# Kernel tuning notes

Hardware: AMD Instinct MI355X
Metric: run time of the kernel (lower is better)

The kernel has to match this reference:

```python
import jax, jax.numpy as jnp
import numpy as np

DIM = 512
NUM_HEADS = 16
D_HEAD = DIM // NUM_HEADS
B, S = 4, 1024


def _relative_shift(pos_score):
    # pos_score: [B, H, S1, S2] -> Transformer-XL relative shift
    b, h, s1, s2 = pos_score.shape
    padded = jnp.pad(pos_score, ((0, 0), (0, 0), (0, 0), (1, 0)))  # [B,H,S1,S2+1]
    padded = padded.reshape(b, h, s2 + 1, s1)
    return padded[:, :, 1:].reshape(b, h, s1, s2)


def setup_inputs() -> dict:
    key = jax.random.key(0)
    ks = jax.random.split(key, 16)
    f32 = jnp.float32
    scale = 0.02
    inp = {
        "query": jax.random.normal(ks[0], (B, S, DIM), f32),
        "key": jax.random.normal(ks[1], (B, S, DIM), f32),
        "value": jax.random.normal(ks[2], (B, S, DIM), f32),
        "pos_embedding": jax.random.normal(ks[3], (B, S, DIM), f32),
        "Wq": jax.random.normal(ks[4], (DIM, DIM), f32) * scale,
        "bq": jnp.zeros((DIM,), f32),
        "Wk": jax.random.normal(ks[5], (DIM, DIM), f32) * scale,
        "bk": jnp.zeros((DIM,), f32),
        "Wv": jax.random.normal(ks[6], (DIM, DIM), f32) * scale,
        "bv": jnp.zeros((DIM,), f32),
        "Wp": jax.random.normal(ks[7], (DIM, DIM), f32) * scale,  # pos_proj, no bias
        "u_bias": jax.random.normal(ks[8], (NUM_HEADS, D_HEAD), f32) * scale,
        "v_bias": jax.random.normal(ks[9], (NUM_HEADS, D_HEAD), f32) * scale,
        "Wo": jax.random.normal(ks[10], (DIM, DIM), f32) * scale,
        "bo": jnp.zeros((DIM,), f32),
    }
    return inp


def reference(query, key, value, pos_embedding, Wq, bq, Wk, bk, Wv, bv, Wp,
              u_bias, v_bias, Wo, bo):
    b = query.shape[0]
    # projections (torch Linear: x @ W.T + b), split heads -> [B, S, H, Dh]
    q = (query @ Wq.T + bq).reshape(b, -1, NUM_HEADS, D_HEAD)
    k = (key @ Wk.T + bk).reshape(b, -1, NUM_HEADS, D_HEAD)
    v = (value @ Wv.T + bv).reshape(b, -1, NUM_HEADS, D_HEAD)
    p = (pos_embedding @ Wp.T).reshape(b, -1, NUM_HEADS, D_HEAD)

    # content score: (q + u) @ k^T  -> [B, H, Sq, Sk]
    content_score = jnp.einsum('bqhd,bkhd->bhqk', q + u_bias, k)
    # position score: (q + v) @ pos^T, then relative shift
    pos_score = jnp.einsum('bqhd,bkhd->bhqk', q + v_bias, p)
    pos_score = _relative_shift(pos_score)

    score = (content_score + pos_score) / np.sqrt(D_HEAD).astype(np.float32)
    attn = jax.nn.softmax(score, axis=-1)  # dropout_p = 0.0 -> identity

    context = jnp.einsum('bhqk,bkhd->bqhd', attn, v).reshape(b, -1, DIM)
    return context @ Wo.T + bo
```

## Files before the change

### kernel.cpp

```cpp
#include <hip/hip_runtime.h>
#include <hip/hip_bf16.h>
#include <math.h>


typedef float f32x4 __attribute__((ext_vector_type(4)));
typedef __bf16 bf16x8 __attribute__((ext_vector_type(8)));
typedef __bf16 bf16x2 __attribute__((ext_vector_type(2)));

#define MFMA16(a, b, c) __builtin_amdgcn_mfma_f32_16x16x32_bf16((a), (b), (c), 0, 0, 0)

constexpr int Bb  = 4;
constexpr int S   = 1024;
constexpr int H   = 16;
constexpr int Dh  = 32;
constexpr int DIM = 512;
constexpr float SCALEL2E = 0.25501818637084186f;
constexpr int ZROWS = 3 * S + 16;

constexpr size_t XN = (size_t)Bb * S * DIM;
constexpr size_t WN = (size_t)DIM * DIM;

__device__ inline bf16x8 cvt8(const float* __restrict__ p) {
  f32x4 a = *(const f32x4*)p;
  f32x4 b = *(const f32x4*)(p + 4);
  bf16x8 r;
  r[0] = (__bf16)a[0]; r[1] = (__bf16)a[1]; r[2] = (__bf16)a[2]; r[3] = (__bf16)a[3];
  r[4] = (__bf16)b[0]; r[5] = (__bf16)b[1]; r[6] = (__bf16)b[2]; r[7] = (__bf16)b[3];
  return r;
}

__device__ inline float fexp2(float x) {
  float r;
  asm("v_exp_f32 %0, %1" : "=v"(r) : "v"(x));
  return r;
}

__device__ inline void gload_lds16(const __bf16* g, __bf16* l) {
  __builtin_amdgcn_global_load_lds(
      (const __attribute__((address_space(1))) unsigned int*)g,
      (__attribute__((address_space(3))) unsigned int*)l, 16, 0, 0);
}

__global__ __launch_bounds__(256) void conv_kernel(
    const float* __restrict__ q, const float* __restrict__ k,
    const float* __restrict__ v, const float* __restrict__ p,
    const float* __restrict__ wq, const float* __restrict__ wk,
    const float* __restrict__ wv, const float* __restrict__ wp,
    const float* __restrict__ wo,
    __bf16* __restrict__ xb, __bf16* __restrict__ wb,
    __bf16* __restrict__ phZ)
{
  const int y = blockIdx.y;
  if (y == 9) {
    const int e8 = blockIdx.x * 256 + threadIdx.x;
    if (e8 < 64 * 136 * 4) {
      const int rowIdx = e8 >> 2, chunk = e8 & 3;
      const int bh = rowIdx / 136;
      const int rl = rowIdx - bh * 136;
      const int row = (rl < 72) ? (960 + rl) : (2040 + (rl - 72));
      bf16x8 zz = {};
      *(bf16x8*)(phZ + ((size_t)bh * ZROWS + row) * Dh + chunk * 8) = zz;
    }
    return;
  }
  const float* src;
  size_t n;
  __bf16* dst;
  if (y < 4) {
    src = (y == 0) ? q : (y == 1) ? k : (y == 2) ? v : p;
    n = XN;
    dst = xb + (size_t)y * XN;
  } else {
    const int w = y - 4;
    src = (w == 0) ? wq : (w == 1) ? wk : (w == 2) ? wv : (w == 3) ? wp : wo;
    n = WN;
    dst = wb + (size_t)w * WN;
  }
  const size_t i = ((size_t)blockIdx.x * 256 + threadIdx.x) * 8;
  if (i >= n) return;
  *(bf16x8*)(dst + i) = cvt8(src + i);
}

template <int MODE>
__global__ __launch_bounds__(256) void gemm_kernel(
    const __bf16* __restrict__ xb, const __bf16* __restrict__ wb,
    const __bf16* __restrict__ ctxp,
    const float* __restrict__ bq, const float* __restrict__ bk,
    const float* __restrict__ bv, const float* __restrict__ bo,
    const float* __restrict__ ub, const float* __restrict__ vb,
    __bf16* __restrict__ qu, __bf16* __restrict__ qv,
    __bf16* __restrict__ kk, __bf16* __restrict__ vt,
    __bf16* __restrict__ phZ,
    float* __restrict__ outp)
{
  constexpr int MR = 2;
  constexpr int BM = MR * 32;
  __shared__ __align__(16) __bf16 smem[BM * 64 + 128 * 64];
  __bf16* As = smem;
  __bf16* Bs = smem + BM * 64;
  __bf16* trans = smem;

  const int bid = blockIdx.x;
  const int u = bid >> 3;
  const int by = u & 3;
  const int idx = (bid & 7) + 8 * (u >> 2);
  int bx, z;
  if (MODE == 0) { bx = idx & 63; z = idx >> 6; }
  else           { bx = idx;      z = 4; }

  const __bf16* Ag = (z < 4) ? (xb + (size_t)z * XN) : ctxp;
  const __bf16* Bg = wb + (size_t)z * WN;

  const int tid = threadIdx.x;
  const int wid = tid >> 6;
  const int ln = tid & 63;
  const int lm = ln & 15, lg = ln >> 4;
  const int wr = wid >> 1, wc = wid & 1;
  const int brow = bx * BM;
  const int bcol = by * 128;

  const int srow = ln >> 3;
  const int sc   = ln & 7;

  f32x4 acc[MR][4] = {};

  for (int kt = 0; kt < DIM / 64; ++kt) {
    const int k0 = kt * 64;
#pragma unroll
    for (int i = 0; i < MR; ++i) {
      const int rb = wid * (MR * 8) + i * 8;
      const int r = rb + srow;
      const int cg = sc ^ (r & 7);
      gload_lds16(Ag + (size_t)(brow + r) * DIM + k0 + cg * 8, &As[rb * 64]);
    }
#pragma unroll
    for (int i = 0; i < 4; ++i) {
      const int rb = wid * 32 + i * 8;
      const int r = rb + srow;
      const int cg = sc ^ (r & 7);
      gload_lds16(Bg + (size_t)(bcol + r) * DIM + k0 + cg * 8, &Bs[rb * 64]);
    }
    __syncthreads();

#pragma unroll
    for (int ks = 0; ks < 2; ++ks) {
      bf16x8 a[MR], b[4];
#pragma unroll
      for (int m = 0; m < MR; ++m) {
        const int row = wr * (MR * 16) + m * 16 + lm;
        const int cc = (ks * 4 + lg) ^ (row & 7);
        a[m] = *(const bf16x8*)&As[row * 64 + cc * 8];
      }
#pragma unroll
      for (int n = 0; n < 4; ++n) {
        const int row = wc * 64 + n * 16 + lm;
        const int cc = (ks * 4 + lg) ^ (row & 7);
        b[n] = *(const bf16x8*)&Bs[row * 64 + cc * 8];
      }
#pragma unroll
      for (int m = 0; m < MR; ++m)
#pragma unroll
        for (int n = 0; n < 4; ++n)
          acc[m][n] = MFMA16(a[m], b[n], acc[m][n]);
    }
    __syncthreads();
  }

  if (MODE == 0 && z == 2) {
    const int b = brow >> 10;
    const int sbase = brow & (S - 1);
#pragma unroll
    for (int n = 0; n < 4; ++n) {
      const int dl = wc * 64 + n * 16 + lm;
      const float bias = bv[bcol + dl];
#pragma unroll
      for (int r = 0; r < 4; ++r) {
        const int p = wr * 32 + 2 * (lg * 4 + r);
        bf16x2 pk;
        pk[0] = (__bf16)(acc[0][n][r] + bias);
        pk[1] = (__bf16)(acc[1][n][r] + bias);
        const int base = dl * 64 + (((p >> 3) ^ (dl & 7)) * 8) + (p & 7);
        *(bf16x2*)(trans + base) = pk;
      }
    }
    __syncthreads();
#pragma unroll
    for (int j = 0; j < 2; ++j) {
      const int dl = (tid >> 2) + j * 64;
      const int d = dl & 31, hl = dl >> 5;
      const int cp = (tid & 3) * 2;
      bf16x8 v0 = *(const bf16x8*)(trans + dl * 64 + ((cp ^ (dl & 7)) * 8));
      bf16x8 v1 = *(const bf16x8*)(trans + dl * 64 + (((cp + 1) ^ (dl & 7)) * 8));
      const int bh2 = b * H + (bcol >> 5) + hl;
      __bf16* dst = vt + ((size_t)bh2 * Dh + d) * S + sbase + cp * 8;
      *(bf16x8*)dst = v0;
      *(bf16x8*)(dst + 8) = v1;
    }
    return;
  }

#pragma unroll
  for (int n = 0; n < 4; ++n) {
    const int o = bcol + wc * 64 + n * 16 + lm;
    float bias = 0.f, ubv = 0.f, vbv = 0.f;
    if (z == 0) { bias = bq[o]; ubv = ub[o]; vbv = vb[o]; }
    else if (z == 1) bias = bk[o];
    else if (z == 4) bias = bo[o];
    const int h = o >> 5, d = o & 31;
#pragma unroll
    for (int m = 0; m < MR; ++m) {
#pragma unroll
      for (int r = 0; r < 4; ++r) {
        const int M = brow + wr * (MR * 16) + m * 16 + lg * 4 + r;
        const float val = acc[m][n][r];
        if (z == 4) {
          outp[(size_t)M * DIM + o] = val + bias;
          continue;
        }
        const int b = M >> 10, s = M & (S - 1);
        const int bh = b * H + h;
        if (z == 0) {
          const size_t idx2 = ((size_t)bh * S + s) * Dh + d;
          qu[idx2] = (__bf16)((val + bias + ubv) * SCALEL2E);
          qv[idx2] = (__bf16)((val + bias + vbv) * SCALEL2E);
        } else if (z == 1) {
          kk[((size_t)bh * S + s) * Dh + d] = (__bf16)(val + bias);
        } else {
          phZ[((size_t)bh * ZROWS + (S + 1 + s)) * Dh + d] = (__bf16)val;
        }
      }
    }
  }
}

__global__ __launch_bounds__(256, 4) void attn_kernel(
    const __bf16* __restrict__ qu, const __bf16* __restrict__ qv,
    const __bf16* __restrict__ kk, const __bf16* __restrict__ vt,
    const __bf16* __restrict__ phZ,
    __bf16* __restrict__ ctx)
{
  __shared__ __align__(16) __bf16 kv_lds[4][2][1024];
  __shared__ __align__(16) __bf16 at_all[4][2][16 * 40];

  const int tid = threadIdx.x;
  const int wid = tid >> 6;
  const int l = tid & 63;
  const int lm = l & 15, lg = l >> 4;

  const int bid = blockIdx.x;
  const int bh = (bid & 7) + 8 * ((bid >> 3) & 7);
  const int q0 = (bid >> 6) * 64 + wid * 16;
  const int h = bh & (H - 1), b = bh >> 4;

  const __bf16* qub = qu + (size_t)bh * S * Dh;
  const __bf16* qvb = qv + (size_t)bh * S * Dh;
  const __bf16* kb  = kk + (size_t)bh * S * Dh;
  const __bf16* vtb = vt + (size_t)bh * Dh * S;
  const __bf16* pZb = phZ + (size_t)bh * ZROWS * Dh;
  const __bf16* pAb = pZb + (size_t)(S + 1) * Dh;

  const bf16x8 au  = *(const bf16x8*)(qub + (size_t)(q0 + lm) * Dh + lg * 8);
  const bf16x8 avA = *(const bf16x8*)(qvb + (size_t)(q0 + lm) * Dh + lg * 8);
  const bf16x8 avB = *(const bf16x8*)(qvb + (size_t)(q0 + 1 + lm) * Dh + lg * 8);

  int  slr[4];
  bool prd[4];
#pragma unroll
  for (int r = 0; r < 4; ++r) {
    const int qr = lg * 4 + r;
    slr[r] = (l & 48) | ((lm - qr + 15) & 15);
    prd[r] = (lm <= qr);
  }

  bf16x8 ones8;
#pragma unroll
  for (int i = 0; i < 8; ++i) ones8[i] = (__bf16)1.0f;

  f32x4 cta = {0.f,0.f,0.f,0.f}, ctb = {0.f,0.f,0.f,0.f};
  f32x4 ls  = {0.f,0.f,0.f,0.f};
  const f32x4 zero4 = {0.f,0.f,0.f,0.f};

  const int srow = l >> 2;
  const int scg  = ((l & 3) ^ ((l >> 3) & 3)) * 8;
  auto stage = [&](int kt, int buf) {
    const __bf16* src;
    if (wid == 0)      src = kb  + (size_t)(kt + srow) * Dh + scg;
    else if (wid == 1) src = kb  + (size_t)(kt + 16 + srow) * Dh + scg;
    else if (wid == 2) src = vtb + (size_t)srow * S + kt + scg;
    else               src = vtb + (size_t)(16 + srow) * S + kt + scg;
    gload_lds16(src, &kv_lds[buf][wid >> 1][(wid & 1) * 512]);
  };

  const int cc = (lg ^ ((lm >> 1) & 3)) * 8;

  auto zld = [&](int ktc, int off, bool uB_) -> bf16x8 {
    const int mb = ktc - q0 + (S - 16);
    const __bf16* zb = uB_ ? pZb : pAb;
    return *(const bf16x8*)(zb + (size_t)(mb + off + lm) * Dh + lg * 8);
  };

  auto half = [&](int kt, int tb, __bf16* at,
                  bf16x8 z0, bf16x8 z1, bf16x8 z2, bool uB_) {
    const __bf16* Ks = kv_lds[tb][0];
    const __bf16* Vs = kv_lds[tb][1];
    bf16x8 kf0 = *(const bf16x8*)(Ks + lm * 32 + cc);
    bf16x8 kf1 = *(const bf16x8*)(Ks + (lm + 16) * 32 + cc);
    __builtin_amdgcn_s_setprio(1);
    f32x4 c0 = MFMA16(au, kf0, zero4);
    f32x4 c1 = MFMA16(au, kf1, zero4);
    const bf16x8 av = uB_ ? avB : avA;
    f32x4 pt0 = MFMA16(av, z0, zero4);
    f32x4 pt1 = MFMA16(av, z1, zero4);
    f32x4 pt2 = MFMA16(av, z2, zero4);
    __builtin_amdgcn_s_setprio(0);
    if (uB_ && (kt < q0 + 16)) {
      const int mb = kt - q0 + (S - 16);
      bf16x8 y0 = *(const bf16x8*)(pAb + (size_t)(mb + lm) * Dh + lg * 8);
      bf16x8 y1 = *(const bf16x8*)(pAb + (size_t)(mb + 16 + lm) * Dh + lg * 8);
      bf16x8 y2 = *(const bf16x8*)(pAb + (size_t)(mb + 32 + lm) * Dh + lg * 8);
      pt0 = MFMA16(avA, y0, pt0);
      pt1 = MFMA16(avA, y1, pt1);
      pt2 = MFMA16(avA, y2, pt2);
    }

#pragma unroll
    for (int r = 0; r < 4; ++r) {
      const float v0 = __shfl(pt0[r], slr[r], 64);
      const float v1 = __shfl(pt1[r], slr[r], 64);
      const float v2 = __shfl(pt2[r], slr[r], 64);
      const float s0 = c0[r] + (prd[r] ? v0 : v1);
      const float s1 = c1[r] + (prd[r] ? v1 : v2);
      bf16x2 pp;
      pp[0] = (__bf16)fexp2(s0);
      pp[1] = (__bf16)fexp2(s1);
      *(bf16x2*)(at + (lg * 4 + r) * 40 + 2 * lm) = pp;
    }

    bf16x8 af  = *(const bf16x8*)(at + lm * 40 + lg * 8);
    bf16x8 vf0 = *(const bf16x8*)(Vs + lm * 32 + cc);
    bf16x8 vf1 = *(const bf16x8*)(Vs + (lm + 16) * 32 + cc);
    __builtin_amdgcn_s_setprio(1);
    cta = MFMA16(af, vf0, cta);
    ctb = MFMA16(af, vf1, ctb);
    ls  = MFMA16(af, ones8, ls);
    __builtin_amdgcn_s_setprio(0);
  };

  __bf16* at0 = at_all[wid][0];
  __bf16* at1 = at_all[wid][1];

  bf16x8 zA0, zA1, zA2;
  bool uA = (0 > q0 - 31);
  zA0 = zld(0, 0, uA);
  zA1 = zld(0, 16, uA);
  zA2 = zld(0, 32, uA);
  stage(0, 0);
  stage(32, 1);
  asm volatile("s_waitcnt vmcnt(0)" ::: "memory");
  __builtin_amdgcn_s_barrier();

  for (int kt = 0; kt < S; kt += 64) {
    const int t = kt >> 5;
    stage((kt + 64 < S) ? kt + 64 : kt, (t + 2) & 3);
    stage((kt + 96 < S) ? kt + 96 : kt, (t + 3) & 3);

    const bool uB = ((kt + 32) > q0 - 31);
    bf16x8 zB0;
    if (uB == uA) zB0 = zA2;
    else          zB0 = zld(kt + 32, 0, uB);
    bf16x8 zB1 = zld(kt + 32, 16, uB);
    bf16x8 zB2 = zld(kt + 32, 32, uB);

    half(kt, t & 3, at0, zA0, zA1, zA2, uA);

    const int ktn = (kt + 64 < S) ? kt + 64 : (S - 32);
    const bool uAn = (ktn > q0 - 31);
    zA1 = zld(ktn, 16, uAn);
    zA2 = zld(ktn, 32, uAn);

    half(kt + 32, (t + 1) & 3, at1, zB0, zB1, zB2, uB);

    if (uAn == uB) zA0 = zB2;
    else           zA0 = zld(ktn, 0, uAn);
    uA = uAn;

    asm volatile("s_waitcnt vmcnt(3)" ::: "memory");
    __builtin_amdgcn_s_barrier();
  }

#pragma unroll
  for (int r = 0; r < 4; ++r) {
    const int s0 = q0 + lg * 4 + r;
    const float inv = 1.f / ls[r];
    __bf16* cp = ctx + ((size_t)b * S + s0) * DIM + h * Dh;
    cp[lm]      = (__bf16)(cta[r] * inv);
    cp[16 + lm] = (__bf16)(ctb[r] * inv);
  }
}

extern "C" void kernel_launch(void* const* d_in, const int* in_sizes, int n_in,
                              void* d_out, int out_size, void* d_ws, size_t ws_size,
                              hipStream_t stream) {
  const float* query = (const float*)d_in[0];
  const float* key   = (const float*)d_in[1];
  const float* value = (const float*)d_in[2];
  const float* pos   = (const float*)d_in[3];
  const float* Wq = (const float*)d_in[4];
  const float* bq = (const float*)d_in[5];
  const float* Wk = (const float*)d_in[6];
  const float* bk = (const float*)d_in[7];
  const float* Wv = (const float*)d_in[8];
  const float* bv = (const float*)d_in[9];
  const float* Wp = (const float*)d_in[10];
  const float* ub = (const float*)d_in[11];
  const float* vb = (const float*)d_in[12];
  const float* Wo = (const float*)d_in[13];
  const float* bo = (const float*)d_in[14];
  float* out = (float*)d_out;

  char* ws = (char*)d_ws;
  const size_t MB = 1ull << 20;
  __bf16* xb  = (__bf16*)(ws + 0 * MB);
  __bf16* wb  = (__bf16*)(ws + 16 * MB);
  __bf16* qu  = (__bf16*)(ws + 19 * MB);
  __bf16* qv  = (__bf16*)(ws + 23 * MB);
  __bf16* kk  = (__bf16*)(ws + 27 * MB);
  __bf16* vt  = (__bf16*)(ws + 31 * MB);
  __bf16* phZ = (__bf16*)(ws + 35 * MB);
  __bf16* ctx = (__bf16*)(ws + 48 * MB);

  conv_kernel<<<dim3(1024, 10), dim3(256), 0, stream>>>(
      query, key, value, pos, Wq, Wk, Wv, Wp, Wo, xb, wb, phZ);

  gemm_kernel<0><<<dim3(1024), dim3(256), 0, stream>>>(
      xb, wb, ctx, bq, bk, bv, bo, ub, vb,
      qu, qv, kk, vt, phZ, out);

  attn_kernel<<<dim3(1024), dim3(256), 0, stream>>>(
      qu, qv, kk, vt, phZ, ctx);

  gemm_kernel<1><<<dim3(256), dim3(256), 0, stream>>>(
      xb, wb, ctx, bq, bk, bv, bo, ub, vb,
      qu, qv, kk, vt, phZ, out);
}
```

Baseline: 82.14 us.

## Fuse fp32-to-bf16 activation conversion into projection GEMM A-tile loads

The separate conversion pass that turned the four fp32 activation tensors into bf16 in the workspace is removed. The projection GEMM now reads fp32 query/key/value/pos directly, converts them in registers and writes the swizzled bf16 A tile to LDS. The conversion kernel shrinks to converting only the weights and zeroing the pad rows. This avoids writing and then re-reading a large bf16 intermediate. In exchange, the A-tile loads become synchronous register loads of twice the bytes, and each fp32 row may be fetched by several column blocks.

After: 77.28 us (median of 2 runs). 1.06x faster.

```diff
diff --git a/kernel.cpp b/kernel.cpp
--- a/kernel.cpp
+++ b/kernel.cpp
@@ -42,16 +42,13 @@
 }
 
 __global__ __launch_bounds__(256) void conv_kernel(
-    const float* __restrict__ q, const float* __restrict__ k,
-    const float* __restrict__ v, const float* __restrict__ p,
     const float* __restrict__ wq, const float* __restrict__ wk,
     const float* __restrict__ wv, const float* __restrict__ wp,
     const float* __restrict__ wo,
-    __bf16* __restrict__ xb, __bf16* __restrict__ wb,
-    __bf16* __restrict__ phZ)
+    __bf16* __restrict__ wb, __bf16* __restrict__ phZ)
 {
   const int y = blockIdx.y;
-  if (y == 9) {
+  if (y == 5) {
     const int e8 = blockIdx.x * 256 + threadIdx.x;
     if (e8 < 64 * 136 * 4) {
       const int rowIdx = e8 >> 2, chunk = e8 & 3;
@@ -63,28 +60,19 @@
     }
     return;
   }
-  const float* src;
-  size_t n;
-  __bf16* dst;
-  if (y < 4) {
-    src = (y == 0) ? q : (y == 1) ? k : (y == 2) ? v : p;
-    n = XN;
-    dst = xb + (size_t)y * XN;
-  } else {
-    const int w = y - 4;
-    src = (w == 0) ? wq : (w == 1) ? wk : (w == 2) ? wv : (w == 3) ? wp : wo;
-    n = WN;
-    dst = wb + (size_t)w * WN;
-  }
+  const float* src = (y == 0) ? wq : (y == 1) ? wk : (y == 2) ? wv
+                   : (y == 3) ? wp : wo;
+  __bf16* dst = wb + (size_t)y * WN;
   const size_t i = ((size_t)blockIdx.x * 256 + threadIdx.x) * 8;
-  if (i >= n) return;
+  if (i >= WN) return;
   *(bf16x8*)(dst + i) = cvt8(src + i);
 }
 
 template <int MODE>
 __global__ __launch_bounds__(256) void gemm_kernel(
-    const __bf16* __restrict__ xb, const __bf16* __restrict__ wb,
-    const __bf16* __restrict__ ctxp,
+    const float* __restrict__ xq, const float* __restrict__ xk,
+    const float* __restrict__ xv, const float* __restrict__ xp,
+    const __bf16* __restrict__ wb, const __bf16* __restrict__ ctxp,
     const float* __restrict__ bq, const float* __restrict__ bk,
     const float* __restrict__ bv, const float* __restrict__ bo,
     const float* __restrict__ ub, const float* __restrict__ vb,
@@ -108,7 +96,7 @@
   if (MODE == 0) { bx = idx & 63; z = idx >> 6; }
   else           { bx = idx;      z = 4; }
 
-  const __bf16* Ag = (z < 4) ? (xb + (size_t)z * XN) : ctxp;
+  const float* Axf = (z == 0) ? xq : (z == 1) ? xk : (z == 2) ? xv : xp;
   const __bf16* Bg = wb + (size_t)z * WN;
 
   const int tid = threadIdx.x;
@@ -126,12 +114,22 @@
 
   for (int kt = 0; kt < DIM / 64; ++kt) {
     const int k0 = kt * 64;
-#pragma unroll
-    for (int i = 0; i < MR; ++i) {
-      const int rb = wid * (MR * 8) + i * 8;
-      const int r = rb + srow;
-      const int cg = sc ^ (r & 7);
-      gload_lds16(Ag + (size_t)(brow + r) * DIM + k0 + cg * 8, &As[rb * 64]);
+    if (MODE == 0) {
+      const int rl = wid * 16 + (ln >> 2);
+      const float* Af = Axf + (size_t)(brow + rl) * DIM + k0;
+      const int c0_ = ln & 3;
+      const int c1_ = c0_ + 4;
+      *(bf16x8*)&As[rl * 64 + ((c0_ ^ (rl & 7)) * 8)] = cvt8(Af + c0_ * 8);
+      *(bf16x8*)&As[rl * 64 + ((c1_ ^ (rl & 7)) * 8)] = cvt8(Af + c1_ * 8);
+    } else {
+#pragma unroll
+      for (int i = 0; i < MR; ++i) {
+        const int rb = wid * (MR * 8) + i * 8;
+        const int r = rb + srow;
+        const int cg = sc ^ (r & 7);
+        gload_lds16(ctxp + (size_t)(brow + r) * DIM + k0 + cg * 8,
+                    &As[rb * 64]);
+      }
     }
 #pragma unroll
     for (int i = 0; i < 4; ++i) {
@@ -420,7 +418,6 @@
 
   char* ws = (char*)d_ws;
   const size_t MB = 1ull << 20;
-  __bf16* xb  = (__bf16*)(ws + 0 * MB);
   __bf16* wb  = (__bf16*)(ws + 16 * MB);
   __bf16* qu  = (__bf16*)(ws + 19 * MB);
   __bf16* qv  = (__bf16*)(ws + 23 * MB);
@@ -429,17 +426,17 @@
   __bf16* phZ = (__bf16*)(ws + 35 * MB);
   __bf16* ctx = (__bf16*)(ws + 48 * MB);
 
-  conv_kernel<<<dim3(1024, 10), dim3(256), 0, stream>>>(
-      query, key, value, pos, Wq, Wk, Wv, Wp, Wo, xb, wb, phZ);
+  conv_kernel<<<dim3(136, 6), dim3(256), 0, stream>>>(
+      Wq, Wk, Wv, Wp, Wo, wb, phZ);
 
   gemm_kernel<0><<<dim3(1024), dim3(256), 0, stream>>>(
-      xb, wb, ctx, bq, bk, bv, bo, ub, vb,
+      query, key, value, pos, wb, ctx, bq, bk, bv, bo, ub, vb,
       qu, qv, kk, vt, phZ, out);
 
   attn_kernel<<<dim3(1024), dim3(256), 0, stream>>>(
       qu, qv, kk, vt, phZ, ctx);
 
   gemm_kernel<1><<<dim3(256), dim3(256), 0, stream>>>(
-      xb, wb, ctx, bq, bk, bv, bo, ub, vb,
+      query, key, value, pos, wb, ctx, bq, bk, bv, bo, ub, vb,
       qu, qv, kk, vt, phZ, out);
 }
```
